# Performance work log

Hardware: AMD Instinct MI355X
Metric: run time of the kernel (lower is better)

## Reference

```python
import jax, jax.numpy as jnp
import numpy as np
import math

B, S, D, H = 2, 2048, 2048, 16
DH = D // H  # 128


def _rope(x, cos, sin):
    # x: [b, s, h, dh]; cos/sin: [s, dh//2]
    b, s, h, dh = x.shape
    x2 = x.reshape(b, s, h, dh // 2, 2)
    a, bb = x2[..., 0], x2[..., 1]
    c = cos[None, :, None, :]
    sn = sin[None, :, None, :]
    out = jnp.stack([a * c - bb * sn, a * sn + bb * c], axis=-1)
    return out.reshape(b, s, h, dh)


def setup_inputs() -> dict:
    key = jax.random.key(0)
    ks = jax.random.split(key, 6)
    x = jax.random.normal(ks[0], (B, S, D), dtype=jnp.float32)
    # RoPE frequencies (theta=10000) as cos/sin of shape [S, DH//2]
    inv_freq = 1.0 / (10000.0 ** (np.arange(0, DH, 2, dtype=np.float32) / DH))
    t = np.arange(S, dtype=np.float32)
    ang = jnp.asarray(np.outer(t, inv_freq))  # [S, DH//2]
    freqs_cos = jnp.cos(ang)
    freqs_sin = jnp.sin(ang)
    # causal additive mask [1,1,S,S]
    neg = jnp.finfo(jnp.float32).min
    mask = jnp.where(jnp.tril(jnp.ones((S, S), dtype=bool)), 0.0, neg)[None, None]
    sc = 0.02
    wq = jax.random.normal(ks[1], (D, D), dtype=jnp.float32) * sc
    wk = jax.random.normal(ks[2], (D, D), dtype=jnp.float32) * sc
    wv = jax.random.normal(ks[3], (D, D), dtype=jnp.float32) * sc
    wo = jax.random.normal(ks[4], (D, D), dtype=jnp.float32) * sc
    return {"x": x, "freqs_cos": freqs_cos, "freqs_sin": freqs_sin,
            "mask": mask, "wq": wq, "wk": wk, "wv": wv, "wo": wo}


def reference(x, freqs_cos, freqs_sin, mask, wq, wk, wv, wo):
    b, s, _ = x.shape
    # torch Linear: y = x @ W.T (weights stored [out, in])
    xq = (x @ wq.T).reshape(b, s, H, DH)
    xk = (x @ wk.T).reshape(b, s, H, DH)
    xv = (x @ wv.T).reshape(b, s, H, DH)
    xq = _rope(xq, freqs_cos, freqs_sin)
    xk = _rope(xk, freqs_cos, freqs_sin)
    # [b, h, s, dh]
    q = xq.transpose(0, 2, 1, 3)
    k = xk.transpose(0, 2, 1, 3)
    v = xv.transpose(0, 2, 1, 3)
    scores = jnp.einsum('bhqd,bhkd->bhqk', q, k) / math.sqrt(DH)
    scores = scores + mask
    attn = jax.nn.softmax(scores, axis=-1)  # dropout p=0 (eval)
    out = jnp.einsum('bhqk,bhkd->bhqd', attn, v)
    out = out.transpose(0, 2, 1, 3).reshape(b, s, D)
    return out @ wo.T
```

## Files before the change

kernel.cpp:

```cpp
#include <hip/hip_runtime.h>

#define B_ 2
#define S_ 2048
#define D_ 2048
#define H_ 16
#define DH_ 128

typedef __bf16 bf16_8 __attribute__((ext_vector_type(8)));
typedef __bf16 bf16_4 __attribute__((ext_vector_type(4)));
typedef float f32x4 __attribute__((ext_vector_type(4)));

__device__ __forceinline__ f32x4 mfma16(bf16_8 a, bf16_8 b, f32x4 c) {
  return __builtin_amdgcn_mfma_f32_16x16x32_bf16(a, b, c, 0, 0, 0);
}

__device__ __forceinline__ bf16_8 load8(const float* p) {
  f32x4 a = *(const f32x4*)p;
  f32x4 b = *(const f32x4*)(p + 4);
  bf16_8 r;
  r[0] = (__bf16)a[0]; r[1] = (__bf16)a[1]; r[2] = (__bf16)a[2]; r[3] = (__bf16)a[3];
  r[4] = (__bf16)b[0]; r[5] = (__bf16)b[1]; r[6] = (__bf16)b[2]; r[7] = (__bf16)b[3];
  return r;
}

__device__ __forceinline__ void async16(const __bf16* g, __bf16* l) {
  __builtin_amdgcn_global_load_lds(
      (const __attribute__((address_space(1))) void*)g,
      (__attribute__((address_space(3))) void*)l, 16, 0, 0);
}

__global__ __launch_bounds__(256) void cvt_all(
    const float* __restrict__ x, const float* __restrict__ wq,
    const float* __restrict__ wk, const float* __restrict__ wv,
    const float* __restrict__ wo, __bf16* __restrict__ xb,
    __bf16* __restrict__ wqb, __bf16* __restrict__ wkb,
    __bf16* __restrict__ wvb, __bf16* __restrict__ wob)
{
  const int W8 = (D_ * D_) / 8;
  int i = blockIdx.x * 256 + threadIdx.x;
  if (i < 2 * W8) {
    *(bf16_8*)(xb + (size_t)i * 8) = load8(x + (size_t)i * 8);
  } else {
    int j = i - 2 * W8;
    int sel = j >> 19, off = j & (W8 - 1);
    const float* s = sel == 0 ? wq : sel == 1 ? wk : sel == 2 ? wv : wo;
    __bf16* d = sel == 0 ? wqb : sel == 1 ? wkb : sel == 2 ? wvb : wob;
    *(bf16_8*)(d + (size_t)off * 8) = load8(s + (size_t)off * 8);
  }
}

template <int QA, int QB, typename STG, typename WT>
__device__ __forceinline__ void phase8(
    const __bf16* Ab, const __bf16* Bb, int wsm64, int wsn32, int l16,
    int colx0, int colx1, f32x4 (&acc)[4][4][2], STG&& stg, WT&& wt)
{
  bf16_8 af[4][2], bfr[2][2];
#pragma unroll
  for (int mi = 0; mi < 4; ++mi) {
    const __bf16* ap = Ab + (QA * 128 + wsm64 + mi * 16 + l16) * 64;
    af[mi][0] = *(const bf16_8*)(ap + colx0);
    af[mi][1] = *(const bf16_8*)(ap + colx1);
  }
#pragma unroll
  for (int ni = 0; ni < 2; ++ni) {
    const __bf16* bp = Bb + (QB * 128 + wsn32 + ni * 16 + l16) * 64;
    bfr[ni][0] = *(const bf16_8*)(bp + colx0);
    bfr[ni][1] = *(const bf16_8*)(bp + colx1);
  }
  stg();
  wt();
  __builtin_amdgcn_s_barrier();
  asm volatile("s_waitcnt lgkmcnt(0)" ::: "memory");
  __builtin_amdgcn_s_setprio(1);
#pragma unroll
  for (int mi = 0; mi < 4; ++mi)
#pragma unroll
    for (int ni = 0; ni < 2; ++ni) {
      acc[QA * 2 + QB][mi][ni] = mfma16(af[mi][0], bfr[ni][0], acc[QA * 2 + QB][mi][ni]);
      acc[QA * 2 + QB][mi][ni] = mfma16(af[mi][1], bfr[ni][1], acc[QA * 2 + QB][mi][ni]);
    }
  __builtin_amdgcn_s_setprio(0);
  asm volatile("" ::: "memory");
  __builtin_amdgcn_s_barrier();
  asm volatile("" ::: "memory");
}

__global__ __launch_bounds__(512, 2) void qkv_gemm8(
    const __bf16* __restrict__ A,
    const __bf16* __restrict__ wqb, const __bf16* __restrict__ wkb,
    const __bf16* __restrict__ wvb,
    const float* __restrict__ fc, const float* __restrict__ fs,
    __bf16* __restrict__ Qo, __bf16* __restrict__ Ko, __bf16* __restrict__ Vo)
{
  __shared__ __align__(16) __bf16 smem8[65536];
  const int tid = threadIdx.x;
  const int wave = tid >> 6, lane = tid & 63;
  const int quad = lane >> 4, l16 = lane & 15;
  const int wsm64 = (wave & 1) * 64;
  const int wsn32 = (wave >> 1) * 32;
  const int m0 = blockIdx.y * 256, n0 = blockIdx.x * 256;
  const int wsel = n0 >> 11, nloc = n0 & 2047;
  const __bf16* Wb = wsel == 0 ? wqb : wsel == 1 ? wkb : wvb;

  const int srow = wave * 8 + (lane >> 3);
  const int scol = ((lane & 7) ^ (lane >> 3)) * 8;
  const __bf16* agl = A  + (size_t)(m0 + srow) * 2048 + scol;
  const __bf16* wgl = Wb + (size_t)(nloc + srow) * 2048 + scol;
  const int ldso = wave * 8 * 64;

  const int colx0 = (quad * 8) ^ ((l16 & 7) * 8);
  const int colx1 = colx0 ^ 32;

  f32x4 acc[4][4][2] = {};

  auto SA8 = [&](int kt, int h, int q) {
    async16(agl + (size_t)(h * 128 + q * 64) * 2048 + (size_t)kt * 64,
            smem8 + (kt & 1) * 16384 + (h * 128 + q * 64) * 64 + ldso);
  };
  auto SB8 = [&](int kt, int h, int q) {
    async16(wgl + (size_t)(h * 128 + q * 64) * 2048 + (size_t)kt * 64,
            smem8 + 32768 + (kt & 1) * 16384 + (h * 128 + q * 64) * 64 + ldso);
  };

  SA8(0, 0, 0); SA8(0, 0, 1); SB8(0, 0, 0); SB8(0, 0, 1);
  SA8(0, 1, 0); SA8(0, 1, 1); SB8(0, 1, 0); SB8(0, 1, 1);
  SA8(1, 0, 0); SA8(1, 0, 1); SB8(1, 0, 0); SB8(1, 0, 1);
  asm volatile("s_waitcnt vmcnt(4)" ::: "memory");
  __builtin_amdgcn_s_barrier();
  asm volatile("" ::: "memory");

  const int nG = 2048 / 64;
  for (int g = 0; g < nG; ++g) {
    const __bf16* Ab = smem8 + (g & 1) * 16384;
    const __bf16* Bb = smem8 + 32768 + (g & 1) * 16384;
    phase8<0, 0>(Ab, Bb, wsm64, wsn32, l16, colx0, colx1, acc,
        [&] { if (g + 1 < nG) { SA8(g + 1, 1, 0); SA8(g + 1, 1, 1); } },
        [&] { if (g == nG - 1) asm volatile("s_waitcnt vmcnt(0)" ::: "memory"); });
    phase8<0, 1>(Ab, Bb, wsm64, wsn32, l16, colx0, colx1, acc,
        [&] { if (g + 1 < nG) { SB8(g + 1, 1, 0); SB8(g + 1, 1, 1); } },
        [&] {});
    phase8<1, 0>(Ab, Bb, wsm64, wsn32, l16, colx0, colx1, acc,
        [&] { if (g + 2 < nG) { SA8(g + 2, 0, 0); SA8(g + 2, 0, 1); } },
        [&] {});
    phase8<1, 1>(Ab, Bb, wsm64, wsn32, l16, colx0, colx1, acc,
        [&] { if (g + 2 < nG) { SB8(g + 2, 0, 0); SB8(g + 2, 0, 1); } },
        [&] { asm volatile("s_waitcnt vmcnt(4)" ::: "memory"); });
  }

  if (wsel < 2) {
    const float qscale = wsel == 0 ? 0.08838834764831845f * 1.4426950408889634f
                                   : 1.0f;
    __bf16* O = wsel == 0 ? Qo : Ko;
#pragma unroll
    for (int q = 0; q < 4; ++q)
#pragma unroll
      for (int mi = 0; mi < 4; ++mi)
#pragma unroll
        for (int ni = 0; ni < 2; ++ni)
#pragma unroll
          for (int r = 0; r < 4; ++r) {
            int row = m0 + (q >> 1) * 128 + wsm64 + mi * 16 + quad * 4 + r;
            int col = nloc + (q & 1) * 128 + wsn32 + ni * 16 + l16;
            float self = acc[q][mi][ni][r];
            float oth = __shfl_xor(self, 1);
            int s = row & (S_ - 1);
            int dh = col & (DH_ - 1);
            float c = fc[s * (DH_ / 2) + (dh >> 1)];
            float sn = fs[s * (DH_ / 2) + (dh >> 1)];
            float o = (dh & 1) ? (oth * sn + self * c) : (self * c - oth * sn);
            O[(size_t)row * 2048 + col] = (__bf16)(o * qscale);
          }
  } else {
    auto Ts = (__bf16(*)[264])smem8;
    const int b = m0 >> 11, sb = m0 & (S_ - 1);
#pragma unroll
    for (int p = 0; p < 4; ++p) {
      __syncthreads();
      if ((wsn32 >> 6) == (p & 1)) {
        const int qb = p >> 1;
#pragma unroll
        for (int qa = 0; qa < 2; ++qa)
#pragma unroll
          for (int mi = 0; mi < 4; ++mi)
#pragma unroll
            for (int ni = 0; ni < 2; ++ni) {
              int cl = (wsn32 & 32) + ni * 16 + l16;
              int rl = qa * 128 + wsm64 + mi * 16 + quad * 4;
              bf16_4 pk;
#pragma unroll
              for (int r = 0; r < 4; ++r) pk[r] = (__bf16)acc[qa * 2 + qb][mi][ni][r];
              *(bf16_4*)&Ts[cl][rl] = pk;
            }
      }
      __syncthreads();
      const int h = (nloc + p * 64) >> 7, dh0 = (nloc + p * 64) & (DH_ - 1);
      __bf16* vb = Vo + ((size_t)(b * H_ + h) * DH_ + dh0) * S_ + sb;
#pragma unroll
      for (int i = 0; i < 4; ++i) {
        int dhl = i * 16 + (tid >> 5);
        int sc = (tid & 31) * 8;
        *(bf16_8*)(vb + (size_t)dhl * S_ + sc) = *(const bf16_8*)&Ts[dhl][sc];
      }
    }
  }
}

template <bool WB>
__global__ __launch_bounds__(256) void qkv_gemm(
    const __bf16* __restrict__ A,
    const float* __restrict__ wqf, const float* __restrict__ wkf,
    const float* __restrict__ wvf,
    const __bf16* __restrict__ wqb, const __bf16* __restrict__ wkb,
    const __bf16* __restrict__ wvb,
    const float* __restrict__ fc, const float* __restrict__ fs,
    __bf16* __restrict__ Qo, __bf16* __restrict__ Ko, __bf16* __restrict__ Vo)
{
  constexpr int TILE = 128 * 32;
  constexpr int STAGE_ELEMS = WB ? 4 * TILE : (128 * 32 + 128 * 40);
  constexpr int TS_ELEMS = 64 * 136;
  constexpr int SM_ELEMS = STAGE_ELEMS > TS_ELEMS ? STAGE_ELEMS : TS_ELEMS;
  __shared__ __align__(16) __bf16 smem[SM_ELEMS];

  const int tid = threadIdx.x;
  const int wave = tid >> 6, lane = tid & 63;
  const int quad = lane >> 4, l16 = lane & 15;
  const int m0 = blockIdx.y * 128, n0 = blockIdx.x * 128;
  const int wsel = n0 >> 11, nloc = n0 & 2047;
  const int wm = (wave >> 1) * 64, wn = (wave & 1) * 64;
  const __bf16* agl = A + (size_t)(m0 + wave * 32 + (lane >> 2)) * 2048 + (lane & 3) * 8;
  f32x4 acc[4][4] = {};
  if (WB) {
    const __bf16* Wbp = wsel == 0 ? wqb : wsel == 1 ? wkb : wvb;
    const __bf16* wgl = Wbp + (size_t)(nloc + wave * 32 + (lane >> 2)) * 2048 + (lane & 3) * 8;
    auto STAGE = [&](int k0, int p) {
      __bf16* ab = smem + p * TILE + (wave * 32) * 32;
      __bf16* wb2 = smem + 2 * TILE + p * TILE + (wave * 32) * 32;
      async16(agl + k0,             ab);
      async16(agl + 16 * 2048 + k0, ab + 16 * 32);
      async16(wgl + k0,             wb2);
      async16(wgl + 16 * 2048 + k0, wb2 + 16 * 32);
    };
    STAGE(0, 0);
#pragma unroll 2
    for (int it = 0; it < 64; ++it) {
      const int p = it & 1;
      if (it + 1 < 64) {
        STAGE((it + 1) * 32, p ^ 1);
        asm volatile("s_waitcnt vmcnt(4)" ::: "memory");
      } else {
        asm volatile("s_waitcnt vmcnt(0)" ::: "memory");
      }
      __builtin_amdgcn_s_barrier();
      asm volatile("" ::: "memory");
      const __bf16* Ab = smem + p * TILE;
      const __bf16* Wbuf = smem + 2 * TILE + p * TILE;
      bf16_8 af[4], bfr[4];
      for (int i = 0; i < 4; ++i) {
        af[i]  = *(const bf16_8*)(Ab   + (wm + i * 16 + l16) * 32 + quad * 8);
        bfr[i] = *(const bf16_8*)(Wbuf + (wn + i * 16 + l16) * 32 + quad * 8);
      }
      for (int mi = 0; mi < 4; ++mi)
        for (int ni = 0; ni < 4; ++ni)
          acc[mi][ni] = mfma16(af[mi], bfr[ni], acc[mi][ni]);
      asm volatile("s_waitcnt lgkmcnt(0)" ::: "memory");
      __builtin_amdgcn_s_barrier();
      asm volatile("" ::: "memory");
    }
  } else {
    auto As = (__bf16(*)[32])smem;
    auto Ws = (__bf16(*)[40])(smem + 128 * 32);
    const float* W = wsel == 0 ? wqf : wsel == 1 ? wkf : wvf;
    const int srow = tid >> 1, scol = (tid & 1) * 16;
    const float* wg = W + (size_t)(nloc + srow) * 2048 + scol;
    for (int k0 = 0; k0 < 2048; k0 += 32) {
      __syncthreads();
      async16(agl + k0,             &As[wave * 32][0]);
      async16(agl + 16 * 2048 + k0, &As[wave * 32 + 16][0]);
      *(bf16_8*)&Ws[srow][scol]     = load8(wg + k0);
      *(bf16_8*)&Ws[srow][scol + 8] = load8(wg + k0 + 8);
      __syncthreads();
      bf16_8 af[4], bfr[4];
      for (int i = 0; i < 4; ++i) {
        af[i]  = *(const bf16_8*)&As[wm + i * 16 + l16][quad * 8];
        bfr[i] = *(const bf16_8*)&Ws[wn + i * 16 + l16][quad * 8];
      }
      for (int mi = 0; mi < 4; ++mi)
        for (int ni = 0; ni < 4; ++ni)
          acc[mi][ni] = mfma16(af[mi], bfr[ni], acc[mi][ni]);
    }
  }
  if (wsel < 2) {
    const float qscale = wsel == 0 ? 0.08838834764831845f * 1.4426950408889634f
                                   : 1.0f;
    __bf16* O = wsel == 0 ? Qo : Ko;
    for (int mi = 0; mi < 4; ++mi)
      for (int ni = 0; ni < 4; ++ni)
        for (int r = 0; r < 4; ++r) {
          int row = m0 + wm + mi * 16 + quad * 4 + r;
          int col = nloc + wn + ni * 16 + l16;
          float self = acc[mi][ni][r];
          float oth = __shfl_xor(self, 1);
          int s = row & (S_ - 1);
          int dh = col & (DH_ - 1);
          float c = fc[s * (DH_ / 2) + (dh >> 1)];
          float sn = fs[s * (DH_ / 2) + (dh >> 1)];
          float o = (dh & 1) ? (oth * sn + self * c) : (self * c - oth * sn);
          O[(size_t)row * 2048 + col] = (__bf16)(o * qscale);
        }
  } else {
    auto Ts = (__bf16(*)[136])smem;
    const int b = m0 >> 11, h = nloc >> 7;
    __bf16* vb = Vo + ((size_t)(b * H_ + h) * DH_) * S_ + (m0 & (S_ - 1));
    for (int p = 0; p < 2; ++p) {
      __syncthreads();
      if ((wn >> 6) == p) {
        for (int mi = 0; mi < 4; ++mi)
          for (int ni = 0; ni < 4; ++ni) {
            int cl = ni * 16 + l16;
            int rl = wm + mi * 16 + quad * 4;
            bf16_4 pk;
            for (int r = 0; r < 4; ++r) pk[r] = (__bf16)acc[mi][ni][r];
            *(bf16_4*)&Ts[cl][rl] = pk;
          }
      }
      __syncthreads();
      for (int i = 0; i < 4; ++i) {
        int dh = p * 64 + i * 16 + (tid >> 4);
        int sc = (tid & 15) * 8;
        *(bf16_8*)(vb + (size_t)dh * S_ + sc) = *(const bf16_8*)&Ts[dh - p * 64][sc];
      }
    }
  }
}

template <bool WB>
__global__ __launch_bounds__(256) void out_gemm(
    const __bf16* __restrict__ A, const float* __restrict__ Wf,
    const __bf16* __restrict__ Wb, float* __restrict__ C)
{
  constexpr int TILE = 128 * 32;
  constexpr int SM_ELEMS = WB ? 4 * TILE : (128 * 32 + 128 * 40);
  __shared__ __align__(16) __bf16 smem[SM_ELEMS];
  const int tid = threadIdx.x;
  const int wave = tid >> 6, lane = tid & 63;
  const int quad = lane >> 4, l16 = lane & 15;
  const int m0 = blockIdx.y * 128, n0 = blockIdx.x * 128;
  const int wm = (wave >> 1) * 64, wn = (wave & 1) * 64;
  const __bf16* agl = A + (size_t)(m0 + wave * 32 + (lane >> 2)) * 2048 + (lane & 3) * 8;
  f32x4 acc[4][4] = {};
  if (WB) {
    const __bf16* wgl = Wb + (size_t)(n0 + wave * 32 + (lane >> 2)) * 2048 + (lane & 3) * 8;
    auto STAGE = [&](int k0, int p) {
      __bf16* ab = smem + p * TILE + (wave * 32) * 32;
      __bf16* wb2 = smem + 2 * TILE + p * TILE + (wave * 32) * 32;
      async16(agl + k0,             ab);
      async16(agl + 16 * 2048 + k0, ab + 16 * 32);
      async16(wgl + k0,             wb2);
      async16(wgl + 16 * 2048 + k0, wb2 + 16 * 32);
    };
    STAGE(0, 0);
#pragma unroll 2
    for (int it = 0; it < 64; ++it) {
      const int p = it & 1;
      if (it + 1 < 64) {
        STAGE((it + 1) * 32, p ^ 1);
        asm volatile("s_waitcnt vmcnt(4)" ::: "memory");
      } else {
        asm volatile("s_waitcnt vmcnt(0)" ::: "memory");
      }
      __builtin_amdgcn_s_barrier();
      asm volatile("" ::: "memory");
      const __bf16* Ab = smem + p * TILE;
      const __bf16* Wbuf = smem + 2 * TILE + p * TILE;
      bf16_8 af[4], bfr[4];
      for (int i = 0; i < 4; ++i) {
        af[i]  = *(const bf16_8*)(Ab   + (wm + i * 16 + l16) * 32 + quad * 8);
        bfr[i] = *(const bf16_8*)(Wbuf + (wn + i * 16 + l16) * 32 + quad * 8);
      }
      for (int mi = 0; mi < 4; ++mi)
        for (int ni = 0; ni < 4; ++ni)
          acc[mi][ni] = mfma16(af[mi], bfr[ni], acc[mi][ni]);
      asm volatile("s_waitcnt lgkmcnt(0)" ::: "memory");
      __builtin_amdgcn_s_barrier();
      asm volatile("" ::: "memory");
    }
  } else {
    auto As = (__bf16(*)[32])smem;
    auto Ws = (__bf16(*)[40])(smem + 128 * 32);
    const int srow = tid >> 1, scol = (tid & 1) * 16;
    const float* wg = Wf + (size_t)(n0 + srow) * 2048 + scol;
    for (int k0 = 0; k0 < 2048; k0 += 32) {
      __syncthreads();
      async16(agl + k0,             &As[wave * 32][0]);
      async16(agl + 16 * 2048 + k0, &As[wave * 32 + 16][0]);
      *(bf16_8*)&Ws[srow][scol]     = load8(wg + k0);
      *(bf16_8*)&Ws[srow][scol + 8] = load8(wg + k0 + 8);
      __syncthreads();
      bf16_8 af[4], bfr[4];
      for (int i = 0; i < 4; ++i) {
        af[i]  = *(const bf16_8*)&As[wm + i * 16 + l16][quad * 8];
        bfr[i] = *(const bf16_8*)&Ws[wn + i * 16 + l16][quad * 8];
      }
      for (int mi = 0; mi < 4; ++mi)
        for (int ni = 0; ni < 4; ++ni)
          acc[mi][ni] = mfma16(af[mi], bfr[ni], acc[mi][ni]);
    }
  }
  for (int mi = 0; mi < 4; ++mi)
    for (int ni = 0; ni < 4; ++ni)
      for (int r = 0; r < 4; ++r) {
        int row = m0 + wm + mi * 16 + quad * 4 + r;
        int col = n0 + wn + ni * 16 + l16;
        C[(size_t)row * 2048 + col] = acc[mi][ni][r];
      }
}

__global__ __launch_bounds__(256) void attn_kernel(
    const __bf16* __restrict__ Q, const __bf16* __restrict__ K,
    const __bf16* __restrict__ Vt_g, __bf16* __restrict__ O)
{
  __shared__ __bf16 Ks[2][64 * 128];
  __shared__ __bf16 Vt[128 * 64];
  __shared__ __bf16 Ps[4][32][72];
  const int tid = threadIdx.x;
  const int wave = tid >> 6, lane = tid & 63;
  const int quad = lane >> 4, l16 = lane & 15;
  const int fid = blockIdx.y * gridDim.x + blockIdx.x;
  const int tid_swz = (fid & 7) * 64 + (fid >> 3);
  const int bh = tid_swz >> 4;
  const int qt = 15 - (tid_swz & 15);
  const size_t base = (size_t)(bh >> 4) * S_ * D_ + (size_t)(bh & 15) * DH_;
  const size_t vtb = (size_t)bh * DH_ * S_;
  const int q0 = qt * 128;
  const int wmin = q0 + wave * 32;

  bf16_8 qf[2][4];
  for (int qs = 0; qs < 2; ++qs) {
    int qrow = wmin + qs * 16 + l16;
    for (int kk = 0; kk < 4; ++kk)
      qf[qs][kk] = *(const bf16_8*)(Q + base + (size_t)qrow * D_ + kk * 32 + quad * 8);
  }
  asm volatile("s_waitcnt vmcnt(0)" ::: "memory");

  const int krs = wave * 4 + (lane >> 4);
  const __bf16* kgl = K + base + (size_t)krs * D_ + ((lane & 15) ^ krs) * 8;
  const int vrs = wave * 8 + (lane >> 3);
  const __bf16* vgl = Vt_g + vtb + (size_t)vrs * S_ + ((lane & 7) ^ (lane >> 3)) * 8;

  f32x4 oacc[2][8] = {};
  float lsum[2][4] = {};
  const int nt = 2 * qt + 2;

  for (int p = 0; p < 4; ++p)
    async16(kgl + (size_t)(p * 16) * D_, Ks[0] + (p * 16 + wave * 4) * 128);
  for (int p = 0; p < 4; ++p)
    async16(vgl + (size_t)(p * 32) * S_, Vt + (p * 32 + wave * 8) * 64);

  int cur = 0;
  for (int kt = 0; kt < nt; ++kt) {
    const bool more = (kt + 1 < nt);
    if (more) {
      for (int p = 0; p < 4; ++p)
        async16(kgl + (size_t)((kt + 1) * 64 + p * 16) * D_,
                Ks[cur ^ 1] + (p * 16 + wave * 4) * 128);
      asm volatile("s_waitcnt vmcnt(8)" ::: "memory");
    } else {
      asm volatile("s_waitcnt vmcnt(4)" ::: "memory");
    }
    __builtin_amdgcn_s_barrier();
    asm volatile("" ::: "memory");

    const bool active = (kt * 64 <= wmin + 31);
    if (active) {
      const bool diag = (kt * 64 + 63 > wmin);
      const __bf16* ksb = Ks[cur];
      for (int n = 0; n < 4; ++n) {
        f32x4 s0 = {}, s1 = {};
        __builtin_amdgcn_s_setprio(1);
#pragma unroll
        for (int kk = 0; kk < 4; ++kk) {
          bf16_8 kf = *(const bf16_8*)&ksb[(n * 16 + l16) * 128 + (((kk * 4 + quad) ^ l16) * 8)];
          s0 = mfma16(qf[0][kk], kf, s0);
          s1 = mfma16(qf[1][kk], kf, s1);
        }
        __builtin_amdgcn_s_setprio(0);
#pragma unroll
        for (int qs = 0; qs < 2; ++qs) {
          f32x4 sv = qs ? s1 : s0;
          for (int r = 0; r < 4; ++r) {
            float v = sv[r];
            if (diag) {
              int qr = wmin + qs * 16 + quad * 4 + r;
              if (kt * 64 + n * 16 + l16 > qr) v = -INFINITY;
            }
            float p = exp2f(v);
            lsum[qs][r] += p;
            Ps[wave][qs * 16 + quad * 4 + r][n * 16 + l16] = (__bf16)p;
          }
        }
      }
    }

    if (more) asm volatile("s_waitcnt vmcnt(4)" ::: "memory");
    else      asm volatile("s_waitcnt vmcnt(0)" ::: "memory");
    __builtin_amdgcn_s_barrier();
    asm volatile("" ::: "memory");

    if (active) {
      bf16_8 pf0[2], pf1[2];
      for (int qs = 0; qs < 2; ++qs) {
        pf0[qs] = *(const bf16_8*)&Ps[wave][qs * 16 + l16][quad * 8];
        pf1[qs] = *(const bf16_8*)&Ps[wave][qs * 16 + l16][32 + quad * 8];
      }
      __builtin_amdgcn_s_setprio(1);
#pragma unroll
      for (int nc = 0; nc < 8; ++nc) {
        bf16_8 vf0 = *(const bf16_8*)&Vt[(nc * 16 + l16) * 64 + ((quad ^ (l16 & 7)) * 8)];
        bf16_8 vf1 = *(const bf16_8*)&Vt[(nc * 16 + l16) * 64 + (((quad + 4) ^ (l16 & 7)) * 8)];
        oacc[0][nc] = mfma16(pf0[0], vf0, oacc[0][nc]);
        oacc[0][nc] = mfma16(pf1[0], vf1, oacc[0][nc]);
        oacc[1][nc] = mfma16(pf0[1], vf0, oacc[1][nc]);
        oacc[1][nc] = mfma16(pf1[1], vf1, oacc[1][nc]);
      }
      __builtin_amdgcn_s_setprio(0);
    }

    asm volatile("s_waitcnt lgkmcnt(0)" ::: "memory");
    __builtin_amdgcn_s_barrier();
    asm volatile("" ::: "memory");
    if (more)
      for (int p = 0; p < 4; ++p)
        async16(vgl + (size_t)(p * 32) * S_ + (size_t)(kt + 1) * 64,
                Vt + (p * 32 + wave * 8) * 64);
    cur ^= 1;
  }

  for (int qs = 0; qs < 2; ++qs)
    for (int r = 0; r < 4; ++r) {
      float l = lsum[qs][r];
      l += __shfl_xor(l, 1);
      l += __shfl_xor(l, 2);
      l += __shfl_xor(l, 4);
      l += __shfl_xor(l, 8);
      float rinv = 1.f / l;
      int qr = wmin + qs * 16 + quad * 4 + r;
      for (int nc = 0; nc < 8; ++nc)
        O[base + (size_t)qr * D_ + nc * 16 + l16] = (__bf16)(oacc[qs][nc][r] * rinv);
    }
}

extern "C" void kernel_launch(void* const* d_in, const int* in_sizes, int n_in,
                              void* d_out, int out_size, void* d_ws, size_t ws_size,
                              hipStream_t stream)
{
  const float* x    = (const float*)d_in[0];
  const float* fcos = (const float*)d_in[1];
  const float* fsin = (const float*)d_in[2];
  const float* wq   = (const float*)d_in[4];
  const float* wk   = (const float*)d_in[5];
  const float* wv   = (const float*)d_in[6];
  const float* wo   = (const float*)d_in[7];
  float* out = (float*)d_out;

  const size_t T = (size_t)B_ * S_ * D_;
  const size_t W = (size_t)D_ * D_;
  __bf16* xb  = (__bf16*)d_ws;
  __bf16* qw  = xb + T;
  __bf16* kw  = qw + T;
  __bf16* vt  = kw + T;
  __bf16* wqb = vt + T;
  __bf16* wkb = wqb + W;
  __bf16* wvb = wkb + W;
  __bf16* wob = wvb + W;
  __bf16* ow  = xb;

  const bool wb = ws_size >= (4 * T + 4 * W) * sizeof(__bf16);
  const int W8 = (int)(W / 8);
  cvt_all<<<(wb ? 6 : 2) * W8 / 256, 256, 0, stream>>>(
      x, wq, wk, wv, wo, xb, wqb, wkb, wvb, wob);
  if (wb)
    qkv_gemm8<<<dim3(24, 16), 512, 0, stream>>>(
        xb, wqb, wkb, wvb, fcos, fsin, qw, kw, vt);
  else
    qkv_gemm<false><<<dim3(48, 32), 256, 0, stream>>>(
        xb, wq, wk, wv, nullptr, nullptr, nullptr, fcos, fsin, qw, kw, vt);
  attn_kernel<<<dim3(S_ / 128, B_ * H_), 256, 0, stream>>>(qw, kw, vt, ow);
  if (wb)
    out_gemm<true><<<dim3(16, 32), 256, 0, stream>>>(ow, nullptr, wob, out);
  else
    out_gemm<false><<<dim3(16, 32), 256, 0, stream>>>(ow, wo, nullptr, out);
}
```

Measured before the change: 429.4 us.

## Collapse four-phase QKV GEMM k-loop into one phase per k-tile

Replaces the four sub-phases per 64-wide k-tile, each with its own barriers and partial prefetch, with a single phase. It reads all A and B fragments from LDS up front, issues one barrier, launches the whole prefetch for tile g+2, then runs all 32 MFMAs. This cuts the number of workgroup barriers per k-tile and is meant to reduce synchronisation stalls. In exchange, each wave holds more fragment registers at once, which adds register pressure under the 512x2 launch bound. Global loads are also issued in larger bursts instead of being interleaved with compute.

Result: faster. 419.6 us (-2.3%).

```diff
diff --git a/kernel.cpp b/kernel.cpp
--- a/kernel.cpp
+++ b/kernel.cpp
@@ -49,42 +49,6 @@
   }
 }
 
-template <int QA, int QB, typename STG, typename WT>
-__device__ __forceinline__ void phase8(
-    const __bf16* Ab, const __bf16* Bb, int wsm64, int wsn32, int l16,
-    int colx0, int colx1, f32x4 (&acc)[4][4][2], STG&& stg, WT&& wt)
-{
-  bf16_8 af[4][2], bfr[2][2];
-#pragma unroll
-  for (int mi = 0; mi < 4; ++mi) {
-    const __bf16* ap = Ab + (QA * 128 + wsm64 + mi * 16 + l16) * 64;
-    af[mi][0] = *(const bf16_8*)(ap + colx0);
-    af[mi][1] = *(const bf16_8*)(ap + colx1);
-  }
-#pragma unroll
-  for (int ni = 0; ni < 2; ++ni) {
-    const __bf16* bp = Bb + (QB * 128 + wsn32 + ni * 16 + l16) * 64;
-    bfr[ni][0] = *(const bf16_8*)(bp + colx0);
-    bfr[ni][1] = *(const bf16_8*)(bp + colx1);
-  }
-  stg();
-  wt();
-  __builtin_amdgcn_s_barrier();
-  asm volatile("s_waitcnt lgkmcnt(0)" ::: "memory");
-  __builtin_amdgcn_s_setprio(1);
-#pragma unroll
-  for (int mi = 0; mi < 4; ++mi)
-#pragma unroll
-    for (int ni = 0; ni < 2; ++ni) {
-      acc[QA * 2 + QB][mi][ni] = mfma16(af[mi][0], bfr[ni][0], acc[QA * 2 + QB][mi][ni]);
-      acc[QA * 2 + QB][mi][ni] = mfma16(af[mi][1], bfr[ni][1], acc[QA * 2 + QB][mi][ni]);
-    }
-  __builtin_amdgcn_s_setprio(0);
-  asm volatile("" ::: "memory");
-  __builtin_amdgcn_s_barrier();
-  asm volatile("" ::: "memory");
-}
-
 __global__ __launch_bounds__(512, 2) void qkv_gemm8(
     const __bf16* __restrict__ A,
     const __bf16* __restrict__ wqb, const __bf16* __restrict__ wkb,
@@ -121,11 +85,14 @@
     async16(wgl + (size_t)(h * 128 + q * 64) * 2048 + (size_t)kt * 64,
             smem8 + 32768 + (kt & 1) * 16384 + (h * 128 + q * 64) * 64 + ldso);
   };
-
-  SA8(0, 0, 0); SA8(0, 0, 1); SB8(0, 0, 0); SB8(0, 0, 1);
-  SA8(0, 1, 0); SA8(0, 1, 1); SB8(0, 1, 0); SB8(0, 1, 1);
-  SA8(1, 0, 0); SA8(1, 0, 1); SB8(1, 0, 0); SB8(1, 0, 1);
-  asm volatile("s_waitcnt vmcnt(4)" ::: "memory");
+  auto STAGE_GRP = [&](int kt) {
+    SA8(kt, 0, 0); SA8(kt, 0, 1); SA8(kt, 1, 0); SA8(kt, 1, 1);
+    SB8(kt, 0, 0); SB8(kt, 0, 1); SB8(kt, 1, 0); SB8(kt, 1, 1);
+  };
+
+  STAGE_GRP(0);
+  STAGE_GRP(1);
+  asm volatile("s_waitcnt vmcnt(8)" ::: "memory");
   __builtin_amdgcn_s_barrier();
   asm volatile("" ::: "memory");
 
@@ -133,18 +100,73 @@
   for (int g = 0; g < nG; ++g) {
     const __bf16* Ab = smem8 + (g & 1) * 16384;
     const __bf16* Bb = smem8 + 32768 + (g & 1) * 16384;
-    phase8<0, 0>(Ab, Bb, wsm64, wsn32, l16, colx0, colx1, acc,
-        [&] { if (g + 1 < nG) { SA8(g + 1, 1, 0); SA8(g + 1, 1, 1); } },
-        [&] { if (g == nG - 1) asm volatile("s_waitcnt vmcnt(0)" ::: "memory"); });
-    phase8<0, 1>(Ab, Bb, wsm64, wsn32, l16, colx0, colx1, acc,
-        [&] { if (g + 1 < nG) { SB8(g + 1, 1, 0); SB8(g + 1, 1, 1); } },
-        [&] {});
-    phase8<1, 0>(Ab, Bb, wsm64, wsn32, l16, colx0, colx1, acc,
-        [&] { if (g + 2 < nG) { SA8(g + 2, 0, 0); SA8(g + 2, 0, 1); } },
-        [&] {});
-    phase8<1, 1>(Ab, Bb, wsm64, wsn32, l16, colx0, colx1, acc,
-        [&] { if (g + 2 < nG) { SB8(g + 2, 0, 0); SB8(g + 2, 0, 1); } },
-        [&] { asm volatile("s_waitcnt vmcnt(4)" ::: "memory"); });
+    bf16_8 af0[4][2], af1[4][2], b0[2][2], b1[2][2];
+
+#pragma unroll
+    for (int mi = 0; mi < 4; ++mi) {
+      const __bf16* ap = Ab + (wsm64 + mi * 16 + l16) * 64;
+      af0[mi][0] = *(const bf16_8*)(ap + colx0);
+      af0[mi][1] = *(const bf16_8*)(ap + colx1);
+    }
+#pragma unroll
+    for (int ni = 0; ni < 2; ++ni) {
+      const __bf16* bp = Bb + (wsn32 + ni * 16 + l16) * 64;
+      b0[ni][0] = *(const bf16_8*)(bp + colx0);
+      b0[ni][1] = *(const bf16_8*)(bp + colx1);
+    }
+#pragma unroll
+    for (int ni = 0; ni < 2; ++ni) {
+      const __bf16* bp = Bb + (128 + wsn32 + ni * 16 + l16) * 64;
+      b1[ni][0] = *(const bf16_8*)(bp + colx0);
+      b1[ni][1] = *(const bf16_8*)(bp + colx1);
+    }
+#pragma unroll
+    for (int mi = 0; mi < 4; ++mi) {
+      const __bf16* ap = Ab + (128 + wsm64 + mi * 16 + l16) * 64;
+      af1[mi][0] = *(const bf16_8*)(ap + colx0);
+      af1[mi][1] = *(const bf16_8*)(ap + colx1);
+    }
+    asm volatile("s_waitcnt lgkmcnt(0)" ::: "memory");
+    __builtin_amdgcn_s_barrier();
+    asm volatile("" ::: "memory");
+
+    if (g + 2 < nG) STAGE_GRP(g + 2);
+
+    __builtin_amdgcn_s_setprio(1);
+#pragma unroll
+    for (int mi = 0; mi < 4; ++mi)
+#pragma unroll
+      for (int ni = 0; ni < 2; ++ni) {
+        acc[0][mi][ni] = mfma16(af0[mi][0], b0[ni][0], acc[0][mi][ni]);
+        acc[0][mi][ni] = mfma16(af0[mi][1], b0[ni][1], acc[0][mi][ni]);
+      }
+#pragma unroll
+    for (int mi = 0; mi < 4; ++mi)
+#pragma unroll
+      for (int ni = 0; ni < 2; ++ni) {
+        acc[1][mi][ni] = mfma16(af0[mi][0], b1[ni][0], acc[1][mi][ni]);
+        acc[1][mi][ni] = mfma16(af0[mi][1], b1[ni][1], acc[1][mi][ni]);
+      }
+#pragma unroll
+    for (int mi = 0; mi < 4; ++mi)
+#pragma unroll
+      for (int ni = 0; ni < 2; ++ni) {
+        acc[2][mi][ni] = mfma16(af1[mi][0], b0[ni][0], acc[2][mi][ni]);
+        acc[2][mi][ni] = mfma16(af1[mi][1], b0[ni][1], acc[2][mi][ni]);
+      }
+#pragma unroll
+    for (int mi = 0; mi < 4; ++mi)
+#pragma unroll
+      for (int ni = 0; ni < 2; ++ni) {
+        acc[3][mi][ni] = mfma16(af1[mi][0], b1[ni][0], acc[3][mi][ni]);
+        acc[3][mi][ni] = mfma16(af1[mi][1], b1[ni][1], acc[3][mi][ni]);
+      }
+    __builtin_amdgcn_s_setprio(0);
+
+    if (g + 2 < nG)      asm volatile("s_waitcnt vmcnt(8)" ::: "memory");
+    else if (g + 1 < nG) asm volatile("s_waitcnt vmcnt(0)" ::: "memory");
+    __builtin_amdgcn_s_barrier();
+    asm volatile("" ::: "memory");
   }
 
   if (wsel < 2) {
```

## Shrink QKV GEMM tile to 256x128 with single-phase double-buffered K loop

Applied to the files above, without the earlier changes.

The QKV projection GEMM now uses a 256x128 output tile per block instead of 256x256, which doubles the grid to 768 blocks. The four-phase ping-pong schedule is replaced by one load-compute step per 64-wide K slice, with prefetch two slices ahead. Each wave now owns a 64x64 sub-tile, and shared memory drops from 128KB to 96KB. The goal is better CU occupancy and wave balance on the device. The cost is lower arithmetic intensity per block and less overlap inside each K step.

New measurement: 411.0 us. 4.3% less time.

```diff
diff --git a/kernel.cpp b/kernel.cpp
--- a/kernel.cpp
+++ b/kernel.cpp
@@ -49,42 +49,6 @@
   }
 }
 
-template <int QA, int QB, typename STG, typename WT>
-__device__ __forceinline__ void phase8(
-    const __bf16* Ab, const __bf16* Bb, int wsm64, int wsn32, int l16,
-    int colx0, int colx1, f32x4 (&acc)[4][4][2], STG&& stg, WT&& wt)
-{
-  bf16_8 af[4][2], bfr[2][2];
-#pragma unroll
-  for (int mi = 0; mi < 4; ++mi) {
-    const __bf16* ap = Ab + (QA * 128 + wsm64 + mi * 16 + l16) * 64;
-    af[mi][0] = *(const bf16_8*)(ap + colx0);
-    af[mi][1] = *(const bf16_8*)(ap + colx1);
-  }
-#pragma unroll
-  for (int ni = 0; ni < 2; ++ni) {
-    const __bf16* bp = Bb + (QB * 128 + wsn32 + ni * 16 + l16) * 64;
-    bfr[ni][0] = *(const bf16_8*)(bp + colx0);
-    bfr[ni][1] = *(const bf16_8*)(bp + colx1);
-  }
-  stg();
-  wt();
-  __builtin_amdgcn_s_barrier();
-  asm volatile("s_waitcnt lgkmcnt(0)" ::: "memory");
-  __builtin_amdgcn_s_setprio(1);
-#pragma unroll
-  for (int mi = 0; mi < 4; ++mi)
-#pragma unroll
-    for (int ni = 0; ni < 2; ++ni) {
-      acc[QA * 2 + QB][mi][ni] = mfma16(af[mi][0], bfr[ni][0], acc[QA * 2 + QB][mi][ni]);
-      acc[QA * 2 + QB][mi][ni] = mfma16(af[mi][1], bfr[ni][1], acc[QA * 2 + QB][mi][ni]);
-    }
-  __builtin_amdgcn_s_setprio(0);
-  asm volatile("" ::: "memory");
-  __builtin_amdgcn_s_barrier();
-  asm volatile("" ::: "memory");
-}
-
 __global__ __launch_bounds__(512, 2) void qkv_gemm8(
     const __bf16* __restrict__ A,
     const __bf16* __restrict__ wqb, const __bf16* __restrict__ wkb,
@@ -92,59 +56,84 @@
     const float* __restrict__ fc, const float* __restrict__ fs,
     __bf16* __restrict__ Qo, __bf16* __restrict__ Ko, __bf16* __restrict__ Vo)
 {
-  __shared__ __align__(16) __bf16 smem8[65536];
+  __shared__ __align__(16) __bf16 smem8[49152];
   const int tid = threadIdx.x;
   const int wave = tid >> 6, lane = tid & 63;
   const int quad = lane >> 4, l16 = lane & 15;
-  const int wsm64 = (wave & 1) * 64;
-  const int wsn32 = (wave >> 1) * 32;
-  const int m0 = blockIdx.y * 256, n0 = blockIdx.x * 256;
+  const int wave_m = wave >> 1;
+  const int wave_n = wave & 1;
+  const int m0 = blockIdx.y * 256, n0 = blockIdx.x * 128;
   const int wsel = n0 >> 11, nloc = n0 & 2047;
   const __bf16* Wb = wsel == 0 ? wqb : wsel == 1 ? wkb : wvb;
 
-  const int srow = wave * 8 + (lane >> 3);
-  const int scol = ((lane & 7) ^ (lane >> 3)) * 8;
+  const int srow = tid >> 3;
+  const int scol = ((tid & 7) ^ ((tid >> 3) & 7)) * 8;
   const __bf16* agl = A  + (size_t)(m0 + srow) * 2048 + scol;
   const __bf16* wgl = Wb + (size_t)(nloc + srow) * 2048 + scol;
-  const int ldso = wave * 8 * 64;
+  const int ldso = wave * 512;
 
   const int colx0 = (quad * 8) ^ ((l16 & 7) * 8);
   const int colx1 = colx0 ^ 32;
 
-  f32x4 acc[4][4][2] = {};
-
-  auto SA8 = [&](int kt, int h, int q) {
-    async16(agl + (size_t)(h * 128 + q * 64) * 2048 + (size_t)kt * 64,
-            smem8 + (kt & 1) * 16384 + (h * 128 + q * 64) * 64 + ldso);
+  f32x4 acc[4][4] = {};
+
+  auto SA = [&](int kt, int q) {
+    async16(agl + (size_t)(q * 64) * 2048 + (size_t)kt * 64,
+            smem8 + (kt & 1) * 16384 + q * 4096 + ldso);
   };
-  auto SB8 = [&](int kt, int h, int q) {
-    async16(wgl + (size_t)(h * 128 + q * 64) * 2048 + (size_t)kt * 64,
-            smem8 + 32768 + (kt & 1) * 16384 + (h * 128 + q * 64) * 64 + ldso);
+  auto SB = [&](int kt, int q) {
+    async16(wgl + (size_t)(q * 64) * 2048 + (size_t)kt * 64,
+            smem8 + 32768 + (kt & 1) * 8192 + q * 4096 + ldso);
   };
-
-  SA8(0, 0, 0); SA8(0, 0, 1); SB8(0, 0, 0); SB8(0, 0, 1);
-  SA8(0, 1, 0); SA8(0, 1, 1); SB8(0, 1, 0); SB8(0, 1, 1);
-  SA8(1, 0, 0); SA8(1, 0, 1); SB8(1, 0, 0); SB8(1, 0, 1);
-  asm volatile("s_waitcnt vmcnt(4)" ::: "memory");
+  auto STAGE_GRP = [&](int kt) {
+    SA(kt, 0); SA(kt, 1); SA(kt, 2); SA(kt, 3);
+    SB(kt, 0); SB(kt, 1);
+  };
+
+  STAGE_GRP(0);
+  STAGE_GRP(1);
+  asm volatile("s_waitcnt vmcnt(6)" ::: "memory");
   __builtin_amdgcn_s_barrier();
   asm volatile("" ::: "memory");
 
   const int nG = 2048 / 64;
   for (int g = 0; g < nG; ++g) {
     const __bf16* Ab = smem8 + (g & 1) * 16384;
-    const __bf16* Bb = smem8 + 32768 + (g & 1) * 16384;
-    phase8<0, 0>(Ab, Bb, wsm64, wsn32, l16, colx0, colx1, acc,
-        [&] { if (g + 1 < nG) { SA8(g + 1, 1, 0); SA8(g + 1, 1, 1); } },
-        [&] { if (g == nG - 1) asm volatile("s_waitcnt vmcnt(0)" ::: "memory"); });
-    phase8<0, 1>(Ab, Bb, wsm64, wsn32, l16, colx0, colx1, acc,
-        [&] { if (g + 1 < nG) { SB8(g + 1, 1, 0); SB8(g + 1, 1, 1); } },
-        [&] {});
-    phase8<1, 0>(Ab, Bb, wsm64, wsn32, l16, colx0, colx1, acc,
-        [&] { if (g + 2 < nG) { SA8(g + 2, 0, 0); SA8(g + 2, 0, 1); } },
-        [&] {});
-    phase8<1, 1>(Ab, Bb, wsm64, wsn32, l16, colx0, colx1, acc,
-        [&] { if (g + 2 < nG) { SB8(g + 2, 0, 0); SB8(g + 2, 0, 1); } },
-        [&] { asm volatile("s_waitcnt vmcnt(4)" ::: "memory"); });
+    const __bf16* Bb = smem8 + 32768 + (g & 1) * 8192;
+    bf16_8 af[4][2], bf[4][2];
+
+#pragma unroll
+    for (int mi = 0; mi < 4; ++mi) {
+      const __bf16* ap = Ab + (wave_m * 64 + mi * 16 + l16) * 64;
+      af[mi][0] = *(const bf16_8*)(ap + colx0);
+      af[mi][1] = *(const bf16_8*)(ap + colx1);
+    }
+#pragma unroll
+    for (int ni = 0; ni < 4; ++ni) {
+      const __bf16* bp = Bb + (wave_n * 64 + ni * 16 + l16) * 64;
+      bf[ni][0] = *(const bf16_8*)(bp + colx0);
+      bf[ni][1] = *(const bf16_8*)(bp + colx1);
+    }
+    asm volatile("s_waitcnt lgkmcnt(0)" ::: "memory");
+    __builtin_amdgcn_s_barrier();
+    asm volatile("" ::: "memory");
+
+    if (g + 2 < nG) STAGE_GRP(g + 2);
+
+    __builtin_amdgcn_s_setprio(1);
+#pragma unroll
+    for (int mi = 0; mi < 4; ++mi)
+#pragma unroll
+      for (int ni = 0; ni < 4; ++ni) {
+        acc[mi][ni] = mfma16(af[mi][0], bf[ni][0], acc[mi][ni]);
+        acc[mi][ni] = mfma16(af[mi][1], bf[ni][1], acc[mi][ni]);
+      }
+    __builtin_amdgcn_s_setprio(0);
+
+    if (g + 2 < nG)      asm volatile("s_waitcnt vmcnt(6)" ::: "memory");
+    else if (g + 1 < nG) asm volatile("s_waitcnt vmcnt(0)" ::: "memory");
+    __builtin_amdgcn_s_barrier();
+    asm volatile("" ::: "memory");
   }
 
   if (wsel < 2) {
@@ -152,49 +141,44 @@
                                    : 1.0f;
     __bf16* O = wsel == 0 ? Qo : Ko;
 #pragma unroll
-    for (int q = 0; q < 4; ++q)
-#pragma unroll
-      for (int mi = 0; mi < 4; ++mi)
-#pragma unroll
-        for (int ni = 0; ni < 2; ++ni)
-#pragma unroll
-          for (int r = 0; r < 4; ++r) {
-            int row = m0 + (q >> 1) * 128 + wsm64 + mi * 16 + quad * 4 + r;
-            int col = nloc + (q & 1) * 128 + wsn32 + ni * 16 + l16;
-            float self = acc[q][mi][ni][r];
-            float oth = __shfl_xor(self, 1);
-            int s = row & (S_ - 1);
-            int dh = col & (DH_ - 1);
-            float c = fc[s * (DH_ / 2) + (dh >> 1)];
-            float sn = fs[s * (DH_ / 2) + (dh >> 1)];
-            float o = (dh & 1) ? (oth * sn + self * c) : (self * c - oth * sn);
-            O[(size_t)row * 2048 + col] = (__bf16)(o * qscale);
-          }
+    for (int mi = 0; mi < 4; ++mi)
+#pragma unroll
+      for (int ni = 0; ni < 4; ++ni)
+#pragma unroll
+        for (int r = 0; r < 4; ++r) {
+          int row = m0 + wave_m * 64 + mi * 16 + quad * 4 + r;
+          int col = nloc + wave_n * 64 + ni * 16 + l16;
+          float self = acc[mi][ni][r];
+          float oth = __shfl_xor(self, 1);
+          int s = row & (S_ - 1);
+          int dh = col & (DH_ - 1);
+          float c = fc[s * (DH_ / 2) + (dh >> 1)];
+          float sn = fs[s * (DH_ / 2) + (dh >> 1)];
+          float o = (dh & 1) ? (oth * sn + self * c) : (self * c - oth * sn);
+          O[(size_t)row * 2048 + col] = (__bf16)(o * qscale);
+        }
   } else {
     auto Ts = (__bf16(*)[264])smem8;
     const int b = m0 >> 11, sb = m0 & (S_ - 1);
-#pragma unroll
-    for (int p = 0; p < 4; ++p) {
-      __syncthreads();
-      if ((wsn32 >> 6) == (p & 1)) {
-        const int qb = p >> 1;
-#pragma unroll
-        for (int qa = 0; qa < 2; ++qa)
-#pragma unroll
-          for (int mi = 0; mi < 4; ++mi)
-#pragma unroll
-            for (int ni = 0; ni < 2; ++ni) {
-              int cl = (wsn32 & 32) + ni * 16 + l16;
-              int rl = qa * 128 + wsm64 + mi * 16 + quad * 4;
-              bf16_4 pk;
-#pragma unroll
-              for (int r = 0; r < 4; ++r) pk[r] = (__bf16)acc[qa * 2 + qb][mi][ni][r];
-              *(bf16_4*)&Ts[cl][rl] = pk;
-            }
-      }
-      __syncthreads();
-      const int h = (nloc + p * 64) >> 7, dh0 = (nloc + p * 64) & (DH_ - 1);
-      __bf16* vb = Vo + ((size_t)(b * H_ + h) * DH_ + dh0) * S_ + sb;
+    const int h = nloc >> 7;
+#pragma unroll
+    for (int p = 0; p < 2; ++p) {
+      __syncthreads();
+      if (wave_n == p) {
+#pragma unroll
+        for (int mi = 0; mi < 4; ++mi)
+#pragma unroll
+          for (int ni = 0; ni < 4; ++ni) {
+            int cl = ni * 16 + l16;
+            int rl = wave_m * 64 + mi * 16 + quad * 4;
+            bf16_4 pk;
+#pragma unroll
+            for (int r = 0; r < 4; ++r) pk[r] = (__bf16)acc[mi][ni][r];
+            *(bf16_4*)&Ts[cl][rl] = pk;
+          }
+      }
+      __syncthreads();
+      __bf16* vb = Vo + ((size_t)(b * H_ + h) * DH_ + p * 64) * S_ + sb;
 #pragma unroll
       for (int i = 0; i < 4; ++i) {
         int dhl = i * 16 + (tid >> 5);
@@ -579,7 +563,7 @@
   cvt_all<<<(wb ? 6 : 2) * W8 / 256, 256, 0, stream>>>(
       x, wq, wk, wv, wo, xb, wqb, wkb, wvb, wob);
   if (wb)
-    qkv_gemm8<<<dim3(24, 16), 512, 0, stream>>>(
+    qkv_gemm8<<<dim3(48, 16), 512, 0, stream>>>(
         xb, wqb, wkb, wvb, fcos, fsin, qw, kw, vt);
   else
     qkv_gemm<false><<<dim3(48, 32), 256, 0, stream>>>(
```
